# Kernel tuning notes

Measured on AMD Instinct MI355X. Metric: run time of the kernel, lower is better.

Reference implementation:

```python
import jax, jax.numpy as jnp
import numpy as np

INTEGRATE_END = 30.0
RTOL, ATOL = 1e-3, 1e-6   # scipy RK45 defaults
MAX_STEPS = 512           # fixed upper bound on adaptive steps (jit-friendly)


def setup_inputs() -> dict:
    key = jax.random.key(0)
    k0, k1, k2, k3, k4 = jax.random.split(key, 5)
    n, perts, T = 4096, 8, 30
    x = jax.random.uniform(k0, (n,), jnp.float32)            # abundances
    r = jax.random.uniform(k1, (n,), jnp.float32)            # growth rates
    eps = jax.random.normal(k2, (n, perts), jnp.float32)     # susceptibilities
    A = jax.random.normal(k3, (n, n), jnp.float32) / (2.0 * n ** 0.5)
    idx = jnp.arange(n)
    A = A.at[idx, idx].set(-1.0)                             # fill_diagonal_(-1)
    P = (jax.random.uniform(k4, (T + 1, perts)) < 0.3).astype(jnp.float32)
    return {"x": x, "t": 30, "r": r, "A": A, "eps": eps, "P": P}


def _integrate(x, t_end, r, A, eps, P):
    T = P.shape[0] - 1

    def f(tc, y):
        # time-dependent perturbation lookup: P[int(T * t / 30)]
        d = jnp.clip((T * tc / INTEGRATE_END).astype(jnp.int32), 0, T)
        return y * (r + A @ y + eps @ P[d])

    def body(carry, _):
        tc, y, h = carry
        h = jnp.minimum(h, t_end - tc)
        active = tc < t_end
        # Dormand-Prince RK45 stages
        k1 = f(tc, y)
        k2 = f(tc + h / 5, y + h * (k1 / 5))
        k3 = f(tc + 3 * h / 10, y + h * (3 / 40 * k1 + 9 / 40 * k2))
        k4 = f(tc + 4 * h / 5, y + h * (44 / 45 * k1 - 56 / 15 * k2 + 32 / 9 * k3))
        k5 = f(tc + 8 * h / 9, y + h * (19372 / 6561 * k1 - 25360 / 2187 * k2
                                        + 64448 / 6561 * k3 - 212 / 729 * k4))
        k6 = f(tc + h, y + h * (9017 / 3168 * k1 - 355 / 33 * k2 + 46732 / 5247 * k3
                                + 49 / 176 * k4 - 5103 / 18656 * k5))
        y5 = y + h * (35 / 384 * k1 + 500 / 1113 * k3 + 125 / 192 * k4
                      - 2187 / 6784 * k5 + 11 / 84 * k6)
        k7 = f(tc + h, y5)
        err = h * (71 / 57600 * k1 - 71 / 16695 * k3 + 71 / 1920 * k4
                   - 17253 / 339200 * k5 + 22 / 525 * k6 - 1 / 40 * k7)
        scale = ATOL + RTOL * jnp.maximum(jnp.abs(y), jnp.abs(y5))
        err_norm = jnp.sqrt(jnp.mean((err / scale) ** 2))
        accept = err_norm <= 1.0
        step = active & accept
        t_new = jnp.where(step, tc + h, tc)
        y_new = jnp.where(step, y5, y)
        factor = jnp.clip(0.9 * (err_norm + 1e-10) ** -0.2, 0.2, 10.0)
        h_new = jnp.where(active, h * factor, h)
        return (t_new, y_new, h_new), None

    h0 = t_end * 0.01
    (tf, yf, hf), _ = jax.lax.scan(body, (jnp.float32(0.0), x, h0), None, length=MAX_STEPS)
    return yf


def reference(x, t, r, A, eps, P):
    t_end = jnp.float32(t)
    return _integrate(x, t_end, r, A, eps, P)
```

## Files before the change

### kernel.cpp

```cpp
#include <hip/hip_runtime.h>
#include <hip/hip_fp16.h>
#include <math.h>


#define N        4096
#define NBLK     256
#define NTHR     256
#define ROWS     16
#define MAXSTEP  512
#define PERTS    8

typedef unsigned long long ull;

static_assert(NBLK * ROWS == N, "row partition");
static_assert(NTHR * 16 == N, "column partition (4 float4 per thread)");

__device__ __forceinline__ float4 ld4(const float* p){ return *reinterpret_cast<const float4*>(p); }
__device__ __forceinline__ void   st4(float* p, float4 v){ *reinterpret_cast<float4*>(p) = v; }

__global__ void __launch_bounds__(NTHR, 1)
mbpert_rk45_kernel(const float* __restrict__ x, const int* __restrict__ tptr,
                   const float* __restrict__ r, const float* __restrict__ A,
                   const float* __restrict__ eps, const float* __restrict__ Pm,
                   float* __restrict__ out, float* __restrict__ W, int Tm)
{
  __shared__ float khist[6][N];
  __shared__ float part_sm[ROWS * 4];
  __shared__ float ys_rows[ROWS];
  __shared__ float ysb_rows[ROWS];
  __shared__ float r_sh[ROWS];
  __shared__ float eps_sh[ROWS * PERTS];
  __shared__ float P_sh[32 * PERTS];
  __shared__ float epr_sh[ROWS];
  __shared__ float es_sh;

  const int tid = threadIdx.x;
  const int b   = blockIdx.x;
  const int rowbase = b * ROWS;
  const int lane = tid & 63;
  const int wv   = tid >> 6;

  unsigned* flags    = reinterpret_cast<unsigned*>(W);
  float*    err_part = W + 256;
  ull*      bword    = reinterpret_cast<ull*>(W + 512);
  ull*      kx0u     = reinterpret_cast<ull*>(W + 1024);
  ull*      kx1u     = reinterpret_cast<ull*>(W + 1024 + N);

  if (tid < ROWS)             r_sh[tid]   = r[rowbase + tid];
  if (tid < ROWS * PERTS)     eps_sh[tid] = eps[rowbase * PERTS + tid];
  if (tid < (Tm + 1) * PERTS) P_sh[tid]   = Pm[tid];
  if (tid < ROWS)             ysb_rows[tid] = x[rowbase + tid];

  __half2 Af[ROWS][8];
  #pragma unroll
  for (int rr = 0; rr < ROWS; rr++){
    const float* Ar = A + (size_t)(rowbase + rr) * N;
    #pragma unroll
    for (int q = 0; q < 4; q++){
      int c = (q * NTHR + tid) * 4;
      float4 a = ld4(Ar + c);
      Af[rr][2*q]   = __floats2half2_rn(a.x, a.y);
      Af[rr][2*q+1] = __floats2half2_rn(a.z, a.w);
    }
  }

  float4 ysbf[4], ysf[4];
  #pragma unroll
  for (int q = 0; q < 4; q++) ysbf[q] = ld4(x + (q * NTHR + tid) * 4);
  __syncthreads();

  const float t_end = (float)(*tptr);
  const float Tf    = (float)Tm;
  float t = 0.0f;
  float h = t_end * 0.01f;
  unsigned gen = 0;

  auto mv = [&](){
    float acc[ROWS];
    #pragma unroll
    for (int rr = 0; rr < ROWS; rr++) acc[rr] = 0.0f;
    #pragma unroll
    for (int q = 0; q < 4; q++){
      float4 y = ysf[q];
      #pragma unroll
      for (int rr = 0; rr < ROWS; rr++){
        float2 lo = __half22float2(Af[rr][2*q]);
        float2 hi = __half22float2(Af[rr][2*q+1]);
        acc[rr] = fmaf(lo.x, y.x, fmaf(lo.y, y.y, fmaf(hi.x, y.z, fmaf(hi.y, y.w, acc[rr]))));
      }
    }
    __syncthreads();
    #pragma unroll
    for (int rr = 0; rr < ROWS; rr++){
      float s = acc[rr];
      #pragma unroll
      for (int off = 32; off; off >>= 1) s += __shfl_xor(s, off, 64);
      if (lane == 0) part_sm[rr * 4 + wv] = s;
    }
    __syncthreads();
  };

  auto kval = [&](float ts) -> float {
    int d = (int)((Tf * ts) / 30.0f);
    d = d < 0 ? 0 : (d > Tm ? Tm : d);
    float dot = part_sm[tid*4] + part_sm[tid*4+1] + part_sm[tid*4+2] + part_sm[tid*4+3];
    float ep = 0.f;
    #pragma unroll
    for (int p = 0; p < PERTS; p++) ep += eps_sh[tid * PERTS + p] * P_sh[d * PERTS + p];
    return ys_rows[tid] * (r_sh[tid] + dot + ep);
  };

  auto build = [&](const int* sli, const float* cf, int nk){
    #pragma unroll
    for (int q = 0; q < 4; q++){
      int c = (q * NTHR + tid) * 4;
      float4 v = ysbf[q];
      for (int m = 0; m < nk; m++){
        float cc = h * cf[m];
        float4 kv = ld4(&khist[sli[m]][c]);
        v.x = fmaf(cc, kv.x, v.x); v.y = fmaf(cc, kv.y, v.y);
        v.z = fmaf(cc, kv.z, v.z); v.w = fmaf(cc, kv.w, v.w);
      }
      ysf[q] = v;
      int o = c - rowbase;
      if (o >= 0 && o < ROWS) st4(&ys_rows[o], v);
    }
    __syncthreads();
  };

  auto publish_flag = [&](float kv, bool werr, float errv) -> ull* {
    ++gen;
    ull* kx = (gen & 1u) ? kx1u : kx0u;
    if (wv == 0){
      float kvn = __shfl_down(kv, 1, 64);
      if ((lane & 1) == 0 && lane < ROWS){
        union { float2 f; ull u; } cv;
        cv.f = make_float2(kv, kvn);
        __hip_atomic_store(&kx[(rowbase >> 1) + (lane >> 1)], cv.u,
                           __ATOMIC_RELAXED, __HIP_MEMORY_SCOPE_AGENT);
      }
      if (werr && lane == 0)
        __hip_atomic_store(&err_part[b], errv, __ATOMIC_RELAXED, __HIP_MEMORY_SCOPE_AGENT);
    }
    __syncthreads();
    if (tid == 0){
      __builtin_amdgcn_sched_barrier(0);
      __builtin_amdgcn_s_waitcnt(0);
      __builtin_amdgcn_sched_barrier(0);
      __hip_atomic_store(&flags[b], gen, __ATOMIC_RELAXED, __HIP_MEMORY_SCOPE_AGENT);
    }
    return kx;
  };

  auto detect = [&](bool werr){
    if (b == 0){
      if (wv == 0){
        for (;;){
          bool ok = true;
          #pragma unroll
          for (int j = 0; j < 4; j++){
            unsigned f = __hip_atomic_load(&flags[j * 64 + lane],
                                           __ATOMIC_RELAXED, __HIP_MEMORY_SCOPE_AGENT);
            ok = ok && (f >= gen);
          }
          if (__all(ok)) break;
          __builtin_amdgcn_s_sleep(2);
        }
        float es = 0.f;
        if (werr){
          #pragma unroll
          for (int j = 0; j < 4; j++)
            es += __hip_atomic_load(&err_part[lane + j * 64],
                                    __ATOMIC_RELAXED, __HIP_MEMORY_SCOPE_AGENT);
          #pragma unroll
          for (int off = 32; off; off >>= 1) es += __shfl_xor(es, off, 64);
        }
        if (lane == 0){
          if (werr) es_sh = es;
          ull pk = ((ull)gen << 32) | (ull)__float_as_uint(es);
          __builtin_amdgcn_sched_barrier(0);
          __builtin_amdgcn_s_waitcnt(0);
          __builtin_amdgcn_sched_barrier(0);
          __hip_atomic_store(bword, pk, __ATOMIC_RELAXED, __HIP_MEMORY_SCOPE_AGENT);
        }
      }
      __syncthreads();
    } else {
      if (tid == 0){
        for (;;){
          ull w = __hip_atomic_load(bword, __ATOMIC_RELAXED, __HIP_MEMORY_SCOPE_AGENT);
          if ((unsigned)(w >> 32) >= gen){
            if (werr) es_sh = __uint_as_float((unsigned)(w & 0xffffffffu));
            break;
          }
          __builtin_amdgcn_s_sleep(2);
        }
      }
      __syncthreads();
    }
  };

  auto exchange = [&](int slot, float kv, bool werr, float errv){
    ull* kx = publish_flag(kv, werr, errv);
    detect(werr);
    float2* kh2 = reinterpret_cast<float2*>(&khist[slot][0]);
    #pragma unroll
    for (int i = 0; i < 8; i++){
      union { float2 f; ull u; } cv;
      cv.u = __hip_atomic_load(&kx[i * NTHR + tid], __ATOMIC_RELAXED, __HIP_MEMORY_SCOPE_AGENT);
      kh2[i * NTHR + tid] = cv.f;
    }
    __syncthreads();
  };

  auto exchange_build = [&](int slot_in, float kv,
                            const int* sli_old, const float* cf_old, int nk_old,
                            float cf_new){
    ull* kx = publish_flag(kv, false, 0.f);
    #pragma unroll
    for (int q = 0; q < 4; q++){
      int c = (q * NTHR + tid) * 4;
      float4 v = ysbf[q];
      for (int m = 0; m < nk_old; m++){
        float cc = h * cf_old[m];
        float4 kvv = ld4(&khist[sli_old[m]][c]);
        v.x = fmaf(cc, kvv.x, v.x); v.y = fmaf(cc, kvv.y, v.y);
        v.z = fmaf(cc, kvv.z, v.z); v.w = fmaf(cc, kvv.w, v.w);
      }
      ysf[q] = v;
    }
    detect(false);
    const float cc = h * cf_new;
    #pragma unroll
    for (int q = 0; q < 4; q++){
      int c = (q * NTHR + tid) * 4;
      union { float2 f; ull u; } c0, c1;
      c0.u = __hip_atomic_load(&kx[(c >> 1)],     __ATOMIC_RELAXED, __HIP_MEMORY_SCOPE_AGENT);
      c1.u = __hip_atomic_load(&kx[(c >> 1) + 1], __ATOMIC_RELAXED, __HIP_MEMORY_SCOPE_AGENT);
      float4 v = ysf[q];
      v.x = fmaf(cc, c0.f.x, v.x); v.y = fmaf(cc, c0.f.y, v.y);
      v.z = fmaf(cc, c1.f.x, v.z); v.w = fmaf(cc, c1.f.y, v.w);
      ysf[q] = v;
      st4(&khist[slot_in][c], make_float4(c0.f.x, c0.f.y, c1.f.x, c1.f.y));
      int o = c - rowbase;
      if (o >= 0 && o < ROWS) st4(&ys_rows[o], v);
    }
  };

  int sl[6] = {0, 1, 2, 3, 4, 5};
  bool exhausted = true;

  for (int n = 0; n < MAXSTEP; ++n){
    if (n > 0){
      float es = es_sh;
      float enorm = sqrtf(es * (1.0f / (float)N));
      bool accept = (enorm <= 1.0f);
      if (accept){
        t += h;
        int tmp = sl[0]; sl[0] = sl[1]; sl[1] = tmp;
        #pragma unroll
        for (int q = 0; q < 4; q++) ysbf[q] = ysf[q];
        if (tid < ROWS) ysb_rows[tid] = ys_rows[tid];
      }
      float fac = 0.9f * powf(enorm + 1e-10f, -0.2f);
      fac = fminf(fmaxf(fac, 0.2f), 10.0f);
      h *= fac;
      __syncthreads();
      if (t >= t_end) { exhausted = false; break; }
      h = fminf(h, t_end - t);
      if (!(h > 0.0f)) { exhausted = false; break; }
      { const float cf[1] = {0.2f}; const int s_[1] = {sl[0]};
        build(s_, cf, 1); }
    } else {
      if (t >= t_end) { exhausted = false; break; }
      h = fminf(h, t_end - t);
      if (!(h > 0.0f)) { exhausted = false; break; }
      #pragma unroll
      for (int q = 0; q < 4; q++){
        ysf[q] = ysbf[q];
        int c = (q * NTHR + tid) * 4, o = c - rowbase;
        if (o >= 0 && o < ROWS) st4(&ys_rows[o], ysf[q]);
      }
      __syncthreads();
      mv();
      float kv = (tid < ROWS) ? kval(t) : 0.f;
      exchange_build(sl[0], kv, nullptr, nullptr, 0, 0.2f);
    }

    mv();
    { float kv = (tid < ROWS) ? kval(t + 0.2f * h) : 0.f;
      const int s_[1] = {sl[0]}; const float cf[1] = {3.f/40.f};
      exchange_build(sl[1], kv, s_, cf, 1, 9.f/40.f); }

    mv();
    { float kv = (tid < ROWS) ? kval(t + 0.3f * h) : 0.f;
      const int s_[2] = {sl[0], sl[1]}; const float cf[2] = {44.f/45.f, -56.f/15.f};
      exchange_build(sl[2], kv, s_, cf, 2, 32.f/9.f); }

    mv();
    { float kv = (tid < ROWS) ? kval(t + 0.8f * h) : 0.f;
      const int s_[3] = {sl[0], sl[1], sl[2]};
      const float cf[3] = {19372.f/6561.f, -25360.f/2187.f, 64448.f/6561.f};
      exchange_build(sl[3], kv, s_, cf, 3, -212.f/729.f); }

    mv();
    { float kv = (tid < ROWS) ? kval(t + (8.f/9.f) * h) : 0.f;
      const int s_[4] = {sl[0], sl[1], sl[2], sl[3]};
      const float cf[4] = {9017.f/3168.f, -355.f/33.f, 46732.f/5247.f, 49.f/176.f};
      exchange_build(sl[4], kv, s_, cf, 4, -5103.f/18656.f); }

    mv();
    { float kv = (tid < ROWS) ? kval(t + h) : 0.f;
      const int s_[4] = {sl[0], sl[2], sl[3], sl[4]};
      const float cf[4] = {35.f/384.f, 500.f/1113.f, 125.f/192.f, -2187.f/6784.f};
      exchange_build(sl[5], kv, s_, cf, 4, 11.f/84.f); }

    mv();
    { float k7v = 0.f, errv = 0.f;
      if (tid < ROWS){
        k7v = kval(t + h);
        int gi = rowbase + tid;
        float e = (71.f/57600.f)  * khist[sl[0]][gi] - (71.f/16695.f)    * khist[sl[2]][gi]
                + (71.f/1920.f)   * khist[sl[3]][gi] - (17253.f/339200.f)* khist[sl[4]][gi]
                + (22.f/525.f)    * khist[sl[5]][gi] - (1.f/40.f)        * k7v;
        e *= h;
        float sc = 1e-6f + 1e-3f * fmaxf(fabsf(ysb_rows[tid]), fabsf(ys_rows[tid]));
        float q = e / sc;
        epr_sh[tid] = q * q;
      }
      __syncthreads();
      if (tid == 0){
        float s = 0.f;
        #pragma unroll
        for (int i = 0; i < ROWS; i++) s += epr_sh[i];
        errv = s;
      }
      exchange(sl[1], k7v, true, errv); }
  }

  if (exhausted){
    float es = es_sh;
    bool accept = sqrtf(es * (1.0f / (float)N)) <= 1.0f;
    if (tid < ROWS) out[rowbase + tid] = accept ? ys_rows[tid] : ysb_rows[tid];
  } else {
    if (tid < ROWS) out[rowbase + tid] = ysb_rows[tid];
  }
}

extern "C" void kernel_launch(void* const* d_in, const int* in_sizes, int n_in,
                              void* d_out, int out_size, void* d_ws, size_t ws_size,
                              hipStream_t stream)
{
  const float* x   = (const float*)d_in[0];
  const int*   tp  = (const int*)  d_in[1];
  const float* r   = (const float*)d_in[2];
  const float* A   = (const float*)d_in[3];
  const float* eps = (const float*)d_in[4];
  const float* Pm  = (const float*)d_in[5];
  float* out = (float*)d_out;
  float* W   = (float*)d_ws;
  int Tm = in_sizes[5] / PERTS - 1;

  hipMemsetAsync(d_ws, 0, 4096, stream);
  mbpert_rk45_kernel<<<dim3(NBLK), dim3(NTHR), 0, stream>>>(
      x, tp, r, A, eps, Pm, out, W, Tm);
}
```

Before: 12.37 ms.

## Replace flag barrier with generation-tagged k-value exchange for RK stages

```diff
diff --git a/kernel.cpp b/kernel.cpp
--- a/kernel.cpp
+++ b/kernel.cpp
@@ -43,8 +43,8 @@
   unsigned* flags    = reinterpret_cast<unsigned*>(W);
   float*    err_part = W + 256;
   ull*      bword    = reinterpret_cast<ull*>(W + 512);
-  ull*      kx0u     = reinterpret_cast<ull*>(W + 1024);
-  ull*      kx1u     = reinterpret_cast<ull*>(W + 1024 + N);
+  ull*      kxt0     = reinterpret_cast<ull*>(W + 1024);
+  ull*      kxt1     = kxt0 + N;
 
   if (tid < ROWS)             r_sh[tid]   = r[rowbase + tid];
   if (tid < ROWS * PERTS)     eps_sh[tid] = eps[rowbase * PERTS + tid];
@@ -73,7 +73,8 @@
   const float Tf    = (float)Tm;
   float t = 0.0f;
   float h = t_end * 0.01f;
-  unsigned gen = 0;
+  unsigned gen  = 0;
+  unsigned sgen = 0;
 
   auto mv = [&](){
     float acc[ROWS];
@@ -128,18 +129,84 @@
     __syncthreads();
   };
 
-  auto publish_flag = [&](float kv, bool werr, float errv) -> ull* {
+  #define TLD(kxt, q, j) __hip_atomic_load(&(kxt)[((q) * NTHR + tid) * 4 + (j)], \
+                                           __ATOMIC_RELAXED, __HIP_MEMORY_SCOPE_AGENT)
+  auto pull_tagged = [&](ull* kxt, ull (&ga)[4][4]){
+    unsigned pend = 0;
+    #pragma unroll
+    for (int q = 0; q < 4; q++)
+      #pragma unroll
+      for (int j = 0; j < 4; j++)
+        ga[q][j] = TLD(kxt, q, j);
+    #pragma unroll
+    for (int q = 0; q < 4; q++)
+      #pragma unroll
+      for (int j = 0; j < 4; j++)
+        if ((unsigned)(ga[q][j] >> 32) != gen) pend |= (1u << (q * 4 + j));
+    while (pend){
+      __builtin_amdgcn_s_sleep(1);
+      #pragma unroll
+      for (int q = 0; q < 4; q++)
+        #pragma unroll
+        for (int j = 0; j < 4; j++){
+          if (pend & (1u << (q * 4 + j))){
+            ull g = TLD(kxt, q, j);
+            if ((unsigned)(g >> 32) == gen){ ga[q][j] = g; pend &= ~(1u << (q * 4 + j)); }
+          }
+        }
+    }
+  };
+
+  auto exchange_build_t = [&](int slot_in, float kv,
+                              const int* sli_old, const float* cf_old, int nk_old,
+                              float cf_new){
     ++gen;
-    ull* kx = (gen & 1u) ? kx1u : kx0u;
+    ull* kxt = (gen & 1u) ? kxt1 : kxt0;
+    if (wv == 0 && lane < ROWS)
+      __hip_atomic_store(&kxt[rowbase + lane],
+                         (((ull)gen) << 32) | (ull)__float_as_uint(kv),
+                         __ATOMIC_RELAXED, __HIP_MEMORY_SCOPE_AGENT);
+    #pragma unroll
+    for (int q = 0; q < 4; q++){
+      int c = (q * NTHR + tid) * 4;
+      float4 v = ysbf[q];
+      for (int m = 0; m < nk_old; m++){
+        float cc = h * cf_old[m];
+        float4 kvv = ld4(&khist[sli_old[m]][c]);
+        v.x = fmaf(cc, kvv.x, v.x); v.y = fmaf(cc, kvv.y, v.y);
+        v.z = fmaf(cc, kvv.z, v.z); v.w = fmaf(cc, kvv.w, v.w);
+      }
+      ysf[q] = v;
+    }
+    ull ga[4][4];
+    pull_tagged(kxt, ga);
+    const float cc = h * cf_new;
+    #pragma unroll
+    for (int q = 0; q < 4; q++){
+      int c = (q * NTHR + tid) * 4;
+      float k0 = __uint_as_float((unsigned)ga[q][0]);
+      float k1 = __uint_as_float((unsigned)ga[q][1]);
+      float k2 = __uint_as_float((unsigned)ga[q][2]);
+      float k3 = __uint_as_float((unsigned)ga[q][3]);
+      float4 v = ysf[q];
+      v.x = fmaf(cc, k0, v.x); v.y = fmaf(cc, k1, v.y);
+      v.z = fmaf(cc, k2, v.z); v.w = fmaf(cc, k3, v.w);
+      ysf[q] = v;
+      st4(&khist[slot_in][c], make_float4(k0, k1, k2, k3));
+      int o = c - rowbase;
+      if (o >= 0 && o < ROWS) st4(&ys_rows[o], v);
+    }
+  };
+
+  auto exchange7 = [&](int slot, float k7v, float errv){
+    ++gen; ++sgen;
+    ull* kxt = (gen & 1u) ? kxt1 : kxt0;
     if (wv == 0){
-      float kvn = __shfl_down(kv, 1, 64);
-      if ((lane & 1) == 0 && lane < ROWS){
-        union { float2 f; ull u; } cv;
-        cv.f = make_float2(kv, kvn);
-        __hip_atomic_store(&kx[(rowbase >> 1) + (lane >> 1)], cv.u,
+      if (lane < ROWS)
+        __hip_atomic_store(&kxt[rowbase + lane],
+                           (((ull)gen) << 32) | (ull)__float_as_uint(k7v),
                            __ATOMIC_RELAXED, __HIP_MEMORY_SCOPE_AGENT);
-      }
-      if (werr && lane == 0)
+      if (lane == 0)
         __hip_atomic_store(&err_part[b], errv, __ATOMIC_RELAXED, __HIP_MEMORY_SCOPE_AGENT);
     }
     __syncthreads();
@@ -147,12 +214,8 @@
       __builtin_amdgcn_sched_barrier(0);
       __builtin_amdgcn_s_waitcnt(0);
       __builtin_amdgcn_sched_barrier(0);
-      __hip_atomic_store(&flags[b], gen, __ATOMIC_RELAXED, __HIP_MEMORY_SCOPE_AGENT);
-    }
-    return kx;
-  };
-
-  auto detect = [&](bool werr){
+      __hip_atomic_store(&flags[b], sgen, __ATOMIC_RELAXED, __HIP_MEMORY_SCOPE_AGENT);
+    }
     if (b == 0){
       if (wv == 0){
         for (;;){
@@ -161,23 +224,21 @@
           for (int j = 0; j < 4; j++){
             unsigned f = __hip_atomic_load(&flags[j * 64 + lane],
                                            __ATOMIC_RELAXED, __HIP_MEMORY_SCOPE_AGENT);
-            ok = ok && (f >= gen);
+            ok = ok && (f >= sgen);
           }
           if (__all(ok)) break;
           __builtin_amdgcn_s_sleep(2);
         }
         float es = 0.f;
-        if (werr){
-          #pragma unroll
-          for (int j = 0; j < 4; j++)
-            es += __hip_atomic_load(&err_part[lane + j * 64],
-                                    __ATOMIC_RELAXED, __HIP_MEMORY_SCOPE_AGENT);
-          #pragma unroll
-          for (int off = 32; off; off >>= 1) es += __shfl_xor(es, off, 64);
-        }
+        #pragma unroll
+        for (int j = 0; j < 4; j++)
+          es += __hip_atomic_load(&err_part[lane + j * 64],
+                                  __ATOMIC_RELAXED, __HIP_MEMORY_SCOPE_AGENT);
+        #pragma unroll
+        for (int off = 32; off; off >>= 1) es += __shfl_xor(es, off, 64);
         if (lane == 0){
-          if (werr) es_sh = es;
-          ull pk = ((ull)gen << 32) | (ull)__float_as_uint(es);
+          es_sh = es;
+          ull pk = ((ull)sgen << 32) | (ull)__float_as_uint(es);
           __builtin_amdgcn_sched_barrier(0);
           __builtin_amdgcn_s_waitcnt(0);
           __builtin_amdgcn_sched_barrier(0);
@@ -189,8 +250,8 @@
       if (tid == 0){
         for (;;){
           ull w = __hip_atomic_load(bword, __ATOMIC_RELAXED, __HIP_MEMORY_SCOPE_AGENT);
-          if ((unsigned)(w >> 32) >= gen){
-            if (werr) es_sh = __uint_as_float((unsigned)(w & 0xffffffffu));
+          if ((unsigned)(w >> 32) >= sgen){
+            es_sh = __uint_as_float((unsigned)(w & 0xffffffffu));
             break;
           }
           __builtin_amdgcn_s_sleep(2);
@@ -198,53 +259,17 @@
       }
       __syncthreads();
     }
-  };
-
-  auto exchange = [&](int slot, float kv, bool werr, float errv){
-    ull* kx = publish_flag(kv, werr, errv);
-    detect(werr);
-    float2* kh2 = reinterpret_cast<float2*>(&khist[slot][0]);
-    #pragma unroll
-    for (int i = 0; i < 8; i++){
-      union { float2 f; ull u; } cv;
-      cv.u = __hip_atomic_load(&kx[i * NTHR + tid], __ATOMIC_RELAXED, __HIP_MEMORY_SCOPE_AGENT);
-      kh2[i * NTHR + tid] = cv.f;
-    }
-    __syncthreads();
-  };
-
-  auto exchange_build = [&](int slot_in, float kv,
-                            const int* sli_old, const float* cf_old, int nk_old,
-                            float cf_new){
-    ull* kx = publish_flag(kv, false, 0.f);
-    #pragma unroll
-    for (int q = 0; q < 4; q++){
-      int c = (q * NTHR + tid) * 4;
-      float4 v = ysbf[q];
-      for (int m = 0; m < nk_old; m++){
-        float cc = h * cf_old[m];
-        float4 kvv = ld4(&khist[sli_old[m]][c]);
-        v.x = fmaf(cc, kvv.x, v.x); v.y = fmaf(cc, kvv.y, v.y);
-        v.z = fmaf(cc, kvv.z, v.z); v.w = fmaf(cc, kvv.w, v.w);
-      }
-      ysf[q] = v;
-    }
-    detect(false);
-    const float cc = h * cf_new;
-    #pragma unroll
-    for (int q = 0; q < 4; q++){
-      int c = (q * NTHR + tid) * 4;
-      union { float2 f; ull u; } c0, c1;
-      c0.u = __hip_atomic_load(&kx[(c >> 1)],     __ATOMIC_RELAXED, __HIP_MEMORY_SCOPE_AGENT);
-      c1.u = __hip_atomic_load(&kx[(c >> 1) + 1], __ATOMIC_RELAXED, __HIP_MEMORY_SCOPE_AGENT);
-      float4 v = ysf[q];
-      v.x = fmaf(cc, c0.f.x, v.x); v.y = fmaf(cc, c0.f.y, v.y);
-      v.z = fmaf(cc, c1.f.x, v.z); v.w = fmaf(cc, c1.f.y, v.w);
-      ysf[q] = v;
-      st4(&khist[slot_in][c], make_float4(c0.f.x, c0.f.y, c1.f.x, c1.f.y));
-      int o = c - rowbase;
-      if (o >= 0 && o < ROWS) st4(&ys_rows[o], v);
-    }
+    ull ga[4][4];
+    pull_tagged(kxt, ga);
+    #pragma unroll
+    for (int q = 0; q < 4; q++){
+      int c = (q * NTHR + tid) * 4;
+      st4(&khist[slot][c], make_float4(__uint_as_float((unsigned)ga[q][0]),
+                                       __uint_as_float((unsigned)ga[q][1]),
+                                       __uint_as_float((unsigned)ga[q][2]),
+                                       __uint_as_float((unsigned)ga[q][3])));
+    }
+    __syncthreads();
   };
 
   int sl[6] = {0, 1, 2, 3, 4, 5};
@@ -284,36 +309,36 @@
       __syncthreads();
       mv();
       float kv = (tid < ROWS) ? kval(t) : 0.f;
-      exchange_build(sl[0], kv, nullptr, nullptr, 0, 0.2f);
+      exchange_build_t(sl[0], kv, nullptr, nullptr, 0, 0.2f);
     }
 
     mv();
     { float kv = (tid < ROWS) ? kval(t + 0.2f * h) : 0.f;
       const int s_[1] = {sl[0]}; const float cf[1] = {3.f/40.f};
-      exchange_build(sl[1], kv, s_, cf, 1, 9.f/40.f); }
+      exchange_build_t(sl[1], kv, s_, cf, 1, 9.f/40.f); }
 
     mv();
     { float kv = (tid < ROWS) ? kval(t + 0.3f * h) : 0.f;
       const int s_[2] = {sl[0], sl[1]}; const float cf[2] = {44.f/45.f, -56.f/15.f};
-      exchange_build(sl[2], kv, s_, cf, 2, 32.f/9.f); }
+      exchange_build_t(sl[2], kv, s_, cf, 2, 32.f/9.f); }
 
     mv();
     { float kv = (tid < ROWS) ? kval(t + 0.8f * h) : 0.f;
       const int s_[3] = {sl[0], sl[1], sl[2]};
       const float cf[3] = {19372.f/6561.f, -25360.f/2187.f, 64448.f/6561.f};
-      exchange_build(sl[3], kv, s_, cf, 3, -212.f/729.f); }
+      exchange_build_t(sl[3], kv, s_, cf, 3, -212.f/729.f); }
 
     mv();
     { float kv = (tid < ROWS) ? kval(t + (8.f/9.f) * h) : 0.f;
       const int s_[4] = {sl[0], sl[1], sl[2], sl[3]};
       const float cf[4] = {9017.f/3168.f, -355.f/33.f, 46732.f/5247.f, 49.f/176.f};
-      exchange_build(sl[4], kv, s_, cf, 4, -5103.f/18656.f); }
+      exchange_build_t(sl[4], kv, s_, cf, 4, -5103.f/18656.f); }
 
     mv();
     { float kv = (tid < ROWS) ? kval(t + h) : 0.f;
       const int s_[4] = {sl[0], sl[2], sl[3], sl[4]};
       const float cf[4] = {35.f/384.f, 500.f/1113.f, 125.f/192.f, -2187.f/6784.f};
-      exchange_build(sl[5], kv, s_, cf, 4, 11.f/84.f); }
+      exchange_build_t(sl[5], kv, s_, cf, 4, 11.f/84.f); }
 
     mv();
     { float k7v = 0.f, errv = 0.f;
@@ -335,7 +360,7 @@
         for (int i = 0; i < ROWS; i++) s += epr_sh[i];
         errv = s;
       }
-      exchange(sl[1], k7v, true, errv); }
+      exchange7(sl[1], k7v, errv); }
   }
 
   if (exhausted){
@@ -361,7 +386,7 @@
   float* W   = (float*)d_ws;
   int Tm = in_sizes[5] / PERTS - 1;
 
-  hipMemsetAsync(d_ws, 0, 4096, stream);
+  hipMemsetAsync(d_ws, 0, 4096 + 2 * (size_t)N * sizeof(ull), stream);
   mbpert_rk45_kernel<<<dim3(NBLK), dim3(NTHR), 0, stream>>>(
       x, tp, r, A, eps, Pm, out, W, Tm);
 }
```

Result: slower. 14.60 ms (+18.1%).
